# Performance work log

Measured on AMD Instinct MI355X. Metric: run time of the kernel, lower is better.

Reference implementation:

```python
import jax, jax.numpy as jnp
import numpy as np

C, FF, NH = 128, 2048, 8
B, D, H, W = 1, 16, 16, 16
EPS = 1e-5

def setup_inputs() -> dict:
    key = jax.random.key(0)
    ks = jax.random.split(key, 20)
    s = 0.02
    inp = {
        'x': jax.random.normal(ks[0], (B, C, D, H, W), jnp.float32),
        'Wq': jax.random.normal(ks[1], (C, C), jnp.float32) * s,
        'bq': jnp.zeros((C,), jnp.float32),
        'Wk': jax.random.normal(ks[2], (C, C), jnp.float32) * s,
        'bk': jnp.zeros((C,), jnp.float32),
        'Wv': jax.random.normal(ks[3], (C, C), jnp.float32) * s,
        'bv': jnp.zeros((C,), jnp.float32),
        'Wo': jax.random.normal(ks[4], (C, C), jnp.float32) * s,
        'bo': jnp.zeros((C,), jnp.float32),
        'W1': jax.random.normal(ks[5], (FF, C), jnp.float32) * s,
        'b1': jnp.zeros((FF,), jnp.float32),
        'W2': jax.random.normal(ks[6], (C, FF), jnp.float32) * s,
        'b2': jnp.zeros((C,), jnp.float32),
        'g1': jnp.ones((C,), jnp.float32),
        'be1': jnp.zeros((C,), jnp.float32),
        'g2': jnp.ones((C,), jnp.float32),
        'be2': jnp.zeros((C,), jnp.float32),
    }
    return inp

def _layernorm(t, g, b):
    # normalize over last (channel) dim, biased variance like torch LayerNorm
    m = jnp.mean(t, axis=-1, keepdims=True)
    v = jnp.mean(jnp.square(t - m), axis=-1, keepdims=True)
    return (t - m) * jax.lax.rsqrt(v + EPS) * g + b

def reference(x, Wq, bq, Wk, bk, Wv, bv, Wo, bo, W1, b1, W2, b2, g1, be1, g2, be2):
    b_, c, d, h, w = x.shape
    n = d * h * w
    hd = c // NH
    xf = x.reshape(b_, c, n)  # [B,C,N]
    # 1x1 conv3d == per-voxel linear over channels
    q = jnp.einsum('oc,bcn->bon', Wq, xf) + bq[:, None]
    k = jnp.einsum('oc,bcn->bon', Wk, xf) + bk[:, None]
    v = jnp.einsum('oc,bcn->bon', Wv, xf) + bv[:, None]
    q = q.reshape(b_, NH, hd, n)
    k = k.reshape(b_, NH, hd, n)
    v = v.reshape(b_, NH, hd, n)
    scores = jnp.einsum('bhcd,bhce->bhde', q, k) / (hd ** 0.5)  # [B,NH,N,N]
    probs = jax.nn.softmax(scores, axis=-1)
    attn = jnp.einsum('bhde,bhce->bhcd', probs, v).reshape(b_, c, n)
    attn = jnp.einsum('oc,bcn->bon', Wo, attn) + bo[:, None]
    x1 = xf + attn  # residual (dropout = identity at eval)
    x1 = _layernorm(x1.transpose(0, 2, 1), g1, be1)  # [B,N,C]
    hmid = jax.nn.relu(jnp.einsum('fc,bnc->bnf', W1, x1) + b1)
    ffn = jnp.einsum('cf,bnf->bnc', W2, hmid) + b2
    x2 = _layernorm(x1 + ffn, g2, be2)
    return x2.transpose(0, 2, 1).reshape(b_, c, d, h, w)
```

## Files before the change

### kernel.cpp

```cpp
#include <hip/hip_runtime.h>
#include <hip/hip_bf16.h>

typedef __hip_bfloat16 bf16;
typedef short short8 __attribute__((ext_vector_type(8)));
typedef float f32x4 __attribute__((ext_vector_type(4)));

#define C_   128
#define N_   4096
#define NH_  8
#define HD_  16
#define FF_  2048
#define SCALE_Q 0.360673760222241f

__device__ __forceinline__ unsigned short f2bf_bits(float f) {
    bf16 h = __float2bfloat16(f);
    return *reinterpret_cast<unsigned short*>(&h);
}
__device__ __forceinline__ float bfs2f(short s) {
    return __uint_as_float(((unsigned int)(unsigned short)s) << 16);
}
__device__ __forceinline__ float fast_exp2(float x) {
    return __builtin_amdgcn_exp2f(x);
}
__device__ __forceinline__ f32x4 mfma16(short8 a, short8 b, f32x4 c) {
    return __builtin_amdgcn_mfma_f32_16x16x32_bf16(a, b, c, 0, 0, 0);
}
__device__ __forceinline__ int kpos(int ko) { return ((ko & 15) << 1) + (ko >> 4); }

__global__ void k_prep(const float* __restrict__ Wq, const float* __restrict__ Wk,
                       const float* __restrict__ Wv, const float* __restrict__ Wo,
                       const float* __restrict__ W1, const float* __restrict__ W2,
                       const float* __restrict__ x,
                       bf16* __restrict__ Wqkvf, bf16* __restrict__ Wof,
                       bf16* __restrict__ W1f, bf16* __restrict__ W2f,
                       bf16* __restrict__ xTf)
{
    const int i = blockIdx.x * 256 + threadIdx.x;
    if (i < 49152) {
        const int o = i >> 7, k = i & 127;
        const float v = (o < 128) ? Wq[i] : (o < 256) ? Wk[i - 16384] : Wv[i - 32768];
        const int pk = kpos(k & 31);
        Wqkvf[(((o >> 4) << 2) + (k >> 5)) * 512 + (((pk >> 3) << 4) + (o & 15)) * 8 + (pk & 7)]
            = __float2bfloat16(v);
    } else if (i < 65536) {
        const int j = i - 49152, o = j >> 7, k = j & 127;
        const int pk = kpos(k & 31);
        Wof[(((o >> 4) << 2) + (k >> 5)) * 512 + (((pk >> 3) << 4) + (o & 15)) * 8 + (pk & 7)]
            = __float2bfloat16(Wo[j]);
    } else if (i < 327680) {
        const int j = i - 65536, o = j >> 7, k = j & 127;
        const int pk = kpos(k & 31);
        W1f[(((o >> 4) << 2) + (k >> 5)) * 512 + (((pk >> 3) << 4) + (o & 15)) * 8 + (pk & 7)]
            = __float2bfloat16(W1[j]);
    } else if (i < 589824) {
        const int j = i - 327680, o = j >> 11, k = j & 2047;
        const int pk = kpos(k & 31);
        W2f[(((o >> 4) << 6) + (k >> 5)) * 512 + (((pk >> 3) << 4) + (o & 15)) * 8 + (pk & 7)]
            = __float2bfloat16(W2[j]);
    } else if (i < 1114112) {
        const int j = i - 589824, c = j >> 12, n = j & 4095;
        const int pk = kpos(c & 31);
        xTf[(((n >> 4) << 2) + (c >> 5)) * 512 + (((pk >> 3) << 4) + (n & 15)) * 8 + (pk & 7)]
            = __float2bfloat16(x[j]);
    }
}

__global__ void __launch_bounds__(256) k_qkv(
    const bf16* __restrict__ xTf, const bf16* __restrict__ Wqkvf,
    const float* __restrict__ bq, const float* __restrict__ bk, const float* __restrict__ bv,
    bf16* __restrict__ qf, bf16* __restrict__ kf, bf16* __restrict__ vf)
{
    const int tid = threadIdx.x, wave = tid >> 6, lane = tid & 63;
    const int col = lane & 15, quad = lane >> 4;
    const int gw = blockIdx.x * 4 + wave;
    const int rt = gw / 24, ct = gw % 24;
    f32x4 acc = {};
    #pragma unroll
    for (int c = 0; c < 4; ++c) {
        short8 a = *(const short8*)(xTf + ((size_t)(rt * 4 + c) << 9) + lane * 8);
        short8 b = *(const short8*)(Wqkvf + ((size_t)(ct * 4 + c) << 9) + lane * 8);
        acc = mfma16(a, b, acc);
    }
    #pragma unroll
    for (int r = 0; r < 4; ++r) {
        const int m = rt * 16 + quad * 4 + r;
        const int n = ct * 16 + col;
        const float v = acc[r];
        if (n < 128) {
            const int h = n >> 4, ch = n & 15;
            qf[((h << 8) + (m >> 4)) * 256 + (((ch >> 3) << 4) + (m & 15)) * 8 + (ch & 7)] =
                __float2bfloat16((v + bq[n]) * SCALE_Q);
        } else if (n < 256) {
            const int c2 = n - 128, h = c2 >> 4, ch = c2 & 15;
            kf[((h << 8) + (m >> 4)) * 256 + (((ch >> 3) << 4) + (m & 15)) * 8 + (ch & 7)] =
                __float2bfloat16(v + bk[c2]);
        } else {
            const int c2 = n - 256, h = c2 >> 4, ch = c2 & 15;
            const int ko = m & 31;
            const int pos = ((ko & 15) << 1) + (ko >> 4);
            vf[((h << 7) + (m >> 5)) * 512 + (((pos >> 3) << 4) + ch) * 8 + (pos & 7)] =
                __float2bfloat16(v + bv[c2]);
        }
    }
}

__global__ void __launch_bounds__(256)
attn_kernel(const bf16* __restrict__ qf, const bf16* __restrict__ kf,
            const bf16* __restrict__ vf, bf16* __restrict__ af)
{
    __shared__ __align__(16) union {
        unsigned int P[4][2][320];
        float comb[4][64][8];
    } sh;
    const int tid = threadIdx.x, wave = tid >> 6, lane = tid & 63;
    const int col = lane & 15, quad = lane >> 4;
    const int gw = blockIdx.x;
    const int h  = gw >> 8;
    const int tile = gw & 255;
    const f32x4 zero = {};

    short8 aq = {};
    if (quad < 2)
        aq = *(const short8*)(qf + ((size_t)((h << 8) + tile) << 8) + lane * 8);

    f32x4 accO = {};
    float L[4] = {0.f, 0.f, 0.f, 0.f};

    const int kbeg = wave << 10;
    for (int i = 0; i < 32; ++i) {
        const int m0 = kbeg + (i << 5);
        unsigned int* Pw = &sh.P[wave][i & 1][0];
        const short* Ps = (const short*)Pw;

        short8 bk0 = {}, bk1 = {};
        if (quad < 2) {
            const bf16* kb = kf + ((size_t)((h << 8) + (m0 >> 4)) << 8) + lane * 8;
            bk0 = *(const short8*)(kb);
            bk1 = *(const short8*)(kb + 256);
        }
        f32x4 s0 = mfma16(aq, bk0, zero);
        f32x4 s1 = mfma16(aq, bk1, zero);
        #pragma unroll
        for (int r = 0; r < 4; ++r) {
            const float p0 = fast_exp2(s0[r]);
            const float p1 = fast_exp2(s1[r]);
            L[r] += p0 + p1;
            Pw[(quad * 4 + r) * 20 + col] =
                ((unsigned int)f2bf_bits(p1) << 16) | f2bf_bits(p0);
        }
        short8 ap = *(const short8*)(Ps + col * 40 + quad * 8);
        short8 bv_ = *(const short8*)(vf + ((size_t)((h << 7) + (m0 >> 5)) << 9) + lane * 8);
        accO = mfma16(ap, bv_, accO);
    }

    __syncthreads();
    #pragma unroll
    for (int r = 0; r < 4; ++r) {
        sh.comb[wave][lane][r]     = accO[r];
        sh.comb[wave][lane][4 + r] = L[r];
    }
    __syncthreads();

    if (wave == 0) {
        #pragma unroll
        for (int r = 0; r < 4; ++r) {
            float O = sh.comb[0][lane][r] + sh.comb[1][lane][r]
                    + sh.comb[2][lane][r] + sh.comb[3][lane][r];
            float l = sh.comb[0][lane][4+r] + sh.comb[1][lane][4+r]
                    + sh.comb[2][lane][4+r] + sh.comb[3][lane][4+r];
            l += __shfl_xor(l, 1); l += __shfl_xor(l, 2);
            l += __shfl_xor(l, 4); l += __shfl_xor(l, 8);
            const int row16 = quad * 4 + r;
            const int pk = (col << 1) + (h & 1);
            af[((tile << 2) + (h >> 1)) * 512 + (((pk >> 3) << 4) + row16) * 8 + (pk & 7)] =
                __float2bfloat16(O / l);
        }
    }
}

__global__ void __launch_bounds__(256, 1)
k_mega(const bf16* __restrict__ af, const bf16* __restrict__ xTf,
       const bf16* __restrict__ Wof, const bf16* __restrict__ W1f, const bf16* __restrict__ W2f,
       const float* __restrict__ bo, const float* __restrict__ b1, const float* __restrict__ b2,
       const float* __restrict__ g1, const float* __restrict__ be1,
       const float* __restrict__ g2, const float* __restrict__ be2,
       float* __restrict__ out)
{
    __shared__ __align__(16) unsigned int Pb[4][2][320];
    __shared__ float comb[96][64];
    const int tid = threadIdx.x, wave = tid >> 6, lane = tid & 63;
    const int col = lane & 15, quad = lane >> 4;
    const int rt = blockIdx.x, n0 = rt << 4;
    const f32x4 zero = {};

    short8 ao[4], xt[4];
    #pragma unroll
    for (int c = 0; c < 4; ++c) {
        ao[c] = *(const short8*)(af  + ((size_t)(rt * 4 + c) << 9) + lane * 8);
        xt[c] = *(const short8*)(xTf + ((size_t)(rt * 4 + c) << 9) + lane * 8);
    }
    f32x4 d[8];
    #pragma unroll
    for (int t = 0; t < 8; ++t) d[t] = zero;
    #pragma unroll
    for (int t = 0; t < 8; ++t)
        #pragma unroll
        for (int c = 0; c < 4; ++c) {
            short8 b = *(const short8*)(Wof + ((size_t)(t * 4 + c) << 9) + lane * 8);
            d[t] = mfma16(ao[c], b, d[t]);
        }
    #pragma unroll
    for (int t = 0; t < 8; ++t) {
        const float bt = bo[t * 16 + col];
        #pragma unroll
        for (int r = 0; r < 4; ++r) d[t][r] += bt;
    }

    float x1f[4][8];
    #pragma unroll
    for (int c = 0; c < 4; ++c) {
        unsigned int* Pw = &Pb[wave][c & 1][0];
        const short* Ps = (const short*)Pw;
        #pragma unroll
        for (int r = 0; r < 4; ++r)
            Pw[(quad * 4 + r) * 20 + col] =
                ((unsigned int)f2bf_bits(d[2 * c + 1][r]) << 16) | f2bf_bits(d[2 * c][r]);
        short8 ar = *(const short8*)(Ps + col * 40 + quad * 8);
        #pragma unroll
        for (int j = 0; j < 8; ++j)
            x1f[c][j] = bfs2f(ar[j]) + bfs2f(xt[c][j]);
    }

    float s = 0.f, ss = 0.f;
    #pragma unroll
    for (int c = 0; c < 4; ++c)
        #pragma unroll
        for (int j = 0; j < 8; ++j) { s += x1f[c][j]; ss += x1f[c][j] * x1f[c][j]; }
    s  += __shfl_xor(s, 16);  s  += __shfl_xor(s, 32);
    ss += __shfl_xor(ss, 16); ss += __shfl_xor(ss, 32);
    const float m1 = s * (1.f / 128.f);
    const float rstd1 = rsqrtf(ss * (1.f / 128.f) - m1 * m1 + 1e-5f);
    short8 aq1[4];
    #pragma unroll
    for (int c = 0; c < 4; ++c)
        #pragma unroll
        for (int j = 0; j < 8; ++j) {
            const int pos = quad * 8 + j;
            const int ko = ((pos & 1) << 4) + (pos >> 1);
            const int ch = c * 32 + ko;
            const float v = (x1f[c][j] - m1) * rstd1 * g1[ch] + be1[ch];
            aq1[c][j] = (short)f2bf_bits(v);
        }

    f32x4 ACC[8];
    #pragma unroll
    for (int t = 0; t < 8; ++t) ACC[t] = zero;
    for (int i = 0; i < 16; ++i) {
        const int ffc = (wave << 4) + i;
        f32x4 p0 = zero, p1 = zero;
        #pragma unroll
        for (int c = 0; c < 4; ++c) {
            short8 b = *(const short8*)(W1f + ((size_t)(ffc * 8 + c) << 9) + lane * 8);
            p0 = mfma16(aq1[c], b, p0);
        }
        #pragma unroll
        for (int c = 0; c < 4; ++c) {
            short8 b = *(const short8*)(W1f + ((size_t)(ffc * 8 + 4 + c) << 9) + lane * 8);
            p1 = mfma16(aq1[c], b, p1);
        }
        const float bb0 = b1[ffc * 32 + col], bb1 = b1[ffc * 32 + 16 + col];
        unsigned int* Pw = &Pb[wave][i & 1][0];
        #pragma unroll
        for (int r = 0; r < 4; ++r) {
            const float v0 = fmaxf(p0[r] + bb0, 0.f);
            const float v1 = fmaxf(p1[r] + bb1, 0.f);
            Pw[(quad * 4 + r) * 20 + col] =
                ((unsigned int)f2bf_bits(v1) << 16) | f2bf_bits(v0);
        }
        short8 ah = *(const short8*)((const short*)Pw + col * 40 + quad * 8);
        #pragma unroll
        for (int t = 0; t < 8; ++t) {
            short8 bw = *(const short8*)(W2f + ((size_t)(t * 64 + ffc) << 9) + lane * 8);
            ACC[t] = mfma16(ah, bw, ACC[t]);
        }
    }

    if (wave) {
        #pragma unroll
        for (int t = 0; t < 8; ++t)
            #pragma unroll
            for (int r = 0; r < 4; ++r)
                comb[(wave - 1) * 32 + t * 4 + r][lane] = ACC[t][r];
    }
    __syncthreads();
    if (wave == 0) {
        #pragma unroll
        for (int t = 0; t < 8; ++t)
            #pragma unroll
            for (int r = 0; r < 4; ++r)
                ACC[t][r] += comb[t * 4 + r][lane] + comb[32 + t * 4 + r][lane]
                           + comb[64 + t * 4 + r][lane];
        short* xb = (short*)&Pb[0][0][0];
        #pragma unroll
        for (int c = 0; c < 4; ++c)
            *(short8*)(xb + (col * 4 + c) * 32 + quad * 8) = aq1[c];
        float t2[8][4];
        #pragma unroll
        for (int t = 0; t < 8; ++t) {
            const int ch = t * 16 + col;
            const int pk = (col << 1) + (t & 1);
            const int c = t >> 1;
            const float bb = b2[ch];
            #pragma unroll
            for (int r = 0; r < 4; ++r)
                t2[t][r] = ACC[t][r] + bb + bfs2f(xb[((quad * 4 + r) * 4 + c) * 32 + pk]);
        }
        #pragma unroll
        for (int r = 0; r < 4; ++r) {
            float S = 0.f, SS = 0.f;
            #pragma unroll
            for (int t = 0; t < 8; ++t) { S += t2[t][r]; SS += t2[t][r] * t2[t][r]; }
            S  += __shfl_xor(S, 1);  S  += __shfl_xor(S, 2);
            S  += __shfl_xor(S, 4);  S  += __shfl_xor(S, 8);
            SS += __shfl_xor(SS, 1); SS += __shfl_xor(SS, 2);
            SS += __shfl_xor(SS, 4); SS += __shfl_xor(SS, 8);
            const float m2 = S * (1.f / 128.f);
            const float rstd2 = rsqrtf(SS * (1.f / 128.f) - m2 * m2 + 1e-5f);
            #pragma unroll
            for (int t = 0; t < 8; ++t) {
                const int ch = t * 16 + col;
                out[(size_t)ch * N_ + n0 + quad * 4 + r] =
                    (t2[t][r] - m2) * rstd2 * g2[ch] + be2[ch];
            }
        }
    }
}

extern "C" void kernel_launch(void* const* d_in, const int* in_sizes, int n_in,
                              void* d_out, int out_size, void* d_ws, size_t ws_size,
                              hipStream_t stream) {
    const float* x   = (const float*)d_in[0];
    const float* Wq  = (const float*)d_in[1];
    const float* bq  = (const float*)d_in[2];
    const float* Wk  = (const float*)d_in[3];
    const float* bk  = (const float*)d_in[4];
    const float* Wv  = (const float*)d_in[5];
    const float* bv  = (const float*)d_in[6];
    const float* Wo  = (const float*)d_in[7];
    const float* bo  = (const float*)d_in[8];
    const float* W1  = (const float*)d_in[9];
    const float* b1  = (const float*)d_in[10];
    const float* W2  = (const float*)d_in[11];
    const float* b2  = (const float*)d_in[12];
    const float* g1  = (const float*)d_in[13];
    const float* be1 = (const float*)d_in[14];
    const float* g2  = (const float*)d_in[15];
    const float* be2 = (const float*)d_in[16];
    float* out = (float*)d_out;

    char* ws = (char*)d_ws;
    bf16* xTf   = (bf16*)(ws + 0);
    bf16* qf    = (bf16*)(ws + 1048576);
    bf16* kf    = (bf16*)(ws + 2097152);
    bf16* vf    = (bf16*)(ws + 3145728);
    bf16* af    = (bf16*)(ws + 4194304);
    bf16* Wqkvf = (bf16*)(ws + 5242880);
    bf16* Wof   = (bf16*)(ws + 5341184);
    bf16* W1f   = (bf16*)(ws + 5373952);
    bf16* W2f   = (bf16*)(ws + 5898240);

    k_prep<<<4352, 256, 0, stream>>>(Wq, Wk, Wv, Wo, W1, W2, x, Wqkvf, Wof, W1f, W2f, xTf);
    k_qkv<<<1536, 256, 0, stream>>>(xTf, Wqkvf, bq, bk, bv, qf, kf, vf);
    attn_kernel<<<2048, 256, 0, stream>>>(qf, kf, vf, af);
    k_mega<<<256, 256, 0, stream>>>(af, xTf, Wof, W1f, W2f, bo, b1, b2,
                                    g1, be1, g2, be2, out);
}
```

Baseline: 149.8 us.

## Double FFN kernel waves, reduce via LDS atomics, truncate bf16 packing

k_mega now runs 8 waves per block instead of 4. Each wave handles 8 FFN chunks instead of 16, and the per-wave partial sums are combined with shared-memory atomicAdd into a zeroed comb buffer instead of a serial reduction in wave 0. Separately, the rounding fp32-to-bf16 conversions in attention and k_mega are replaced with bit truncation to cut ALU work. The wider block adds more latency hiding for the 256-block grid, at the cost of atomic contention, an extra zeroing pass and barrier, and slightly different numerics from truncation.

```diff
diff --git a/kernel.cpp b/kernel.cpp
--- a/kernel.cpp
+++ b/kernel.cpp
@@ -15,6 +15,12 @@
 __device__ __forceinline__ unsigned short f2bf_bits(float f) {
     bf16 h = __float2bfloat16(f);
     return *reinterpret_cast<unsigned short*>(&h);
+}
+__device__ __forceinline__ unsigned int pack_trunc(float lo, float hi) {
+    return (__float_as_uint(hi) & 0xffff0000u) | (__float_as_uint(lo) >> 16);
+}
+__device__ __forceinline__ short f2bf_trunc(float f) {
+    return (short)(__float_as_uint(f) >> 16);
 }
 __device__ __forceinline__ float bfs2f(short s) {
     return __uint_as_float(((unsigned int)(unsigned short)s) << 16);
@@ -145,8 +151,7 @@
             const float p0 = fast_exp2(s0[r]);
             const float p1 = fast_exp2(s1[r]);
             L[r] += p0 + p1;
-            Pw[(quad * 4 + r) * 20 + col] =
-                ((unsigned int)f2bf_bits(p1) << 16) | f2bf_bits(p0);
+            Pw[(quad * 4 + r) * 20 + col] = pack_trunc(p0, p1);
         }
         short8 ap = *(const short8*)(Ps + col * 40 + quad * 8);
         short8 bv_ = *(const short8*)(vf + ((size_t)((h << 7) + (m0 >> 5)) << 9) + lane * 8);
@@ -178,7 +183,7 @@
     }
 }
 
-__global__ void __launch_bounds__(256, 1)
+__global__ void __launch_bounds__(512, 1)
 k_mega(const bf16* __restrict__ af, const bf16* __restrict__ xTf,
        const bf16* __restrict__ Wof, const bf16* __restrict__ W1f, const bf16* __restrict__ W2f,
        const float* __restrict__ bo, const float* __restrict__ b1, const float* __restrict__ b2,
@@ -186,13 +191,16 @@
        const float* __restrict__ g2, const float* __restrict__ be2,
        float* __restrict__ out)
 {
-    __shared__ __align__(16) unsigned int Pb[4][2][320];
-    __shared__ float comb[96][64];
+    __shared__ __align__(16) unsigned int Pb[8][2][320];
+    __shared__ float comb[32][64];
     const int tid = threadIdx.x, wave = tid >> 6, lane = tid & 63;
     const int col = lane & 15, quad = lane >> 4;
     const int rt = blockIdx.x, n0 = rt << 4;
     const f32x4 zero = {};
 
+    for (int i = tid; i < 2048; i += 512) ((float*)comb)[i] = 0.f;
+    __syncthreads();
+
     short8 ao[4], xt[4];
     #pragma unroll
     for (int c = 0; c < 4; ++c) {
@@ -223,8 +231,7 @@
         const short* Ps = (const short*)Pw;
         #pragma unroll
         for (int r = 0; r < 4; ++r)
-            Pw[(quad * 4 + r) * 20 + col] =
-                ((unsigned int)f2bf_bits(d[2 * c + 1][r]) << 16) | f2bf_bits(d[2 * c][r]);
+            Pw[(quad * 4 + r) * 20 + col] = pack_trunc(d[2 * c][r], d[2 * c + 1][r]);
         short8 ar = *(const short8*)(Ps + col * 40 + quad * 8);
         #pragma unroll
         for (int j = 0; j < 8; ++j)
@@ -248,15 +255,14 @@
             const int pos = quad * 8 + j;
             const int ko = ((pos & 1) << 4) + (pos >> 1);
             const int ch = c * 32 + ko;
-            const float v = (x1f[c][j] - m1) * rstd1 * g1[ch] + be1[ch];
-            aq1[c][j] = (short)f2bf_bits(v);
+            aq1[c][j] = f2bf_trunc((x1f[c][j] - m1) * rstd1 * g1[ch] + be1[ch]);
         }
 
     f32x4 ACC[8];
     #pragma unroll
     for (int t = 0; t < 8; ++t) ACC[t] = zero;
-    for (int i = 0; i < 16; ++i) {
-        const int ffc = (wave << 4) + i;
+    for (int i = 0; i < 8; ++i) {
+        const int ffc = (wave << 3) + i;
         f32x4 p0 = zero, p1 = zero;
         #pragma unroll
         for (int c = 0; c < 4; ++c) {
@@ -271,12 +277,9 @@
         const float bb0 = b1[ffc * 32 + col], bb1 = b1[ffc * 32 + 16 + col];
         unsigned int* Pw = &Pb[wave][i & 1][0];
         #pragma unroll
-        for (int r = 0; r < 4; ++r) {
-            const float v0 = fmaxf(p0[r] + bb0, 0.f);
-            const float v1 = fmaxf(p1[r] + bb1, 0.f);
+        for (int r = 0; r < 4; ++r)
             Pw[(quad * 4 + r) * 20 + col] =
-                ((unsigned int)f2bf_bits(v1) << 16) | f2bf_bits(v0);
-        }
+                pack_trunc(fmaxf(p0[r] + bb0, 0.f), fmaxf(p1[r] + bb1, 0.f));
         short8 ah = *(const short8*)((const short*)Pw + col * 40 + quad * 8);
         #pragma unroll
         for (int t = 0; t < 8; ++t) {
@@ -285,21 +288,13 @@
         }
     }
 
-    if (wave) {
-        #pragma unroll
-        for (int t = 0; t < 8; ++t)
-            #pragma unroll
-            for (int r = 0; r < 4; ++r)
-                comb[(wave - 1) * 32 + t * 4 + r][lane] = ACC[t][r];
-    }
+    #pragma unroll
+    for (int t = 0; t < 8; ++t)
+        #pragma unroll
+        for (int r = 0; r < 4; ++r)
+            atomicAdd(&comb[t * 4 + r][lane], ACC[t][r]);
     __syncthreads();
     if (wave == 0) {
-        #pragma unroll
-        for (int t = 0; t < 8; ++t)
-            #pragma unroll
-            for (int r = 0; r < 4; ++r)
-                ACC[t][r] += comb[t * 4 + r][lane] + comb[32 + t * 4 + r][lane]
-                           + comb[64 + t * 4 + r][lane];
         short* xb = (short*)&Pb[0][0][0];
         #pragma unroll
         for (int c = 0; c < 4; ++c)
@@ -313,7 +308,8 @@
             const float bb = b2[ch];
             #pragma unroll
             for (int r = 0; r < 4; ++r)
-                t2[t][r] = ACC[t][r] + bb + bfs2f(xb[((quad * 4 + r) * 4 + c) * 32 + pk]);
+                t2[t][r] = comb[t * 4 + r][lane] + bb
+                         + bfs2f(xb[((quad * 4 + r) * 4 + c) * 32 + pk]);
         }
         #pragma unroll
         for (int r = 0; r < 4; ++r) {
@@ -372,6 +368,6 @@
     k_prep<<<4352, 256, 0, stream>>>(Wq, Wk, Wv, Wo, W1, W2, x, Wqkvf, Wof, W1f, W2f, xTf);
     k_qkv<<<1536, 256, 0, stream>>>(xTf, Wqkvf, bq, bk, bv, qf, kf, vf);
     attn_kernel<<<2048, 256, 0, stream>>>(qf, kf, vf, af);
-    k_mega<<<256, 256, 0, stream>>>(af, xTf, Wof, W1f, W2f, bo, b1, b2,
+    k_mega<<<256, 512, 0, stream>>>(af, xTf, Wof, W1f, W2f, bo, b1, b2,
                                     g1, be1, g2, be2, out);
 }
```

Result: slower. 167.6 us (+11.9%).
